# Kernel optimization log

Measured on AMD Instinct MI355X. Metric: run time of the kernel, lower is better.

The kernel has to match this reference:

```python
import jax, jax.numpy as jnp
import numpy as np

B, T, DIM = 4, 2048, 512
H = 8
HD = DIM // H  # 64
ALPHA = 100.0
EPS = 1e-10


def setup_inputs() -> dict:
    key = jax.random.key(0)
    k1, k2, k3, k4 = jax.random.split(key, 4)
    x = jax.random.normal(k1, (B, T, DIM), dtype=jnp.float32)
    # torch Linear weights; stored here as [in, out] for x @ W
    W_qkv = jax.random.normal(k2, (DIM, 2 * DIM), dtype=jnp.float32) * (DIM ** -0.5)
    W_proj = jax.random.normal(k3, (DIM, DIM), dtype=jnp.float32) * (DIM ** -0.5)
    b_proj = jax.random.normal(k4, (DIM,), dtype=jnp.float32) * 0.01
    return {"x": x, "W_qkv": W_qkv, "W_proj": W_proj, "b_proj": b_proj}


def reference(x, W_qkv, W_proj, b_proj):
    b, t, dim = x.shape
    qkv = x @ W_qkv                                   # [b,t,2*dim]
    # einops 'b t (d k h) -> k b h t d' with k=2, h=H: innermost grouping order (d, k, h)
    qkv = qkv.reshape(b, t, HD, 2, H)                 # [b,t,d,2,h]
    qk = jnp.transpose(qkv[:, :, :, 0, :], (0, 3, 1, 2))  # [b,h,t,d]
    v = jnp.transpose(qkv[:, :, :, 1, :], (0, 3, 1, 2))   # [b,h,t,d]
    q = qk  # q == k
    qsq = jnp.sum(q * q, axis=-1)                     # [b,h,t]
    dots = jnp.einsum('bhtd,bhsd->bhts', q, q)        # [b,h,t,s]
    score = -(qsq[..., :, None] + qsq[..., None, :] - 2.0 * dots)
    # Frobenius norm of q over (t,d) per (b,h)
    a = jnp.sqrt(jnp.sum(q * q, axis=(2, 3), keepdims=True))  # [b,h,1,1]
    x_norm = jnp.sqrt(jnp.sum(x * x, axis=-1))                 # [b,t]
    bmax = jnp.max(x_norm, axis=1).reshape(b, 1, 1, 1)         # [b,1,1,1]
    scale = 1.0 / (a * bmax + EPS)
    attn = jax.nn.softmax(ALPHA * score * scale, axis=-1)      # [b,h,t,s]
    out = jnp.einsum('bhts,bhsd->bhtd', attn, v)               # [b,h,t,d]
    out = jnp.transpose(out, (0, 2, 1, 3)).reshape(b, t, dim)  # b t (h d)
    return out @ W_proj + b_proj
```

## Files before the change

kernel.cpp:

```cpp
#include <hip/hip_runtime.h>
#include <hip/hip_bf16.h>

#define BB 4
#define TT 2048
#define DIM 512
#define NH 8
#define HD 64
#define NROW (BB*TT)
#define BH (BB*NH)

typedef unsigned short u16;
typedef unsigned int u32;
typedef __attribute__((ext_vector_type(8))) short bf16x8;
typedef __attribute__((ext_vector_type(8))) unsigned short u16x8;
typedef __attribute__((ext_vector_type(4))) float f32x4;
typedef __attribute__((ext_vector_type(16))) float f32x16;
typedef __attribute__((ext_vector_type(4))) unsigned short u16x4;
typedef __attribute__((ext_vector_type(2))) unsigned int u32x2;

static __device__ __forceinline__ float bf2f(u16 u) {
    return __uint_as_float(((u32)u) << 16);
}
static __device__ __forceinline__ u16 f2bf(float f) {
    u32 u = __float_as_uint(f);
    u32 r = (u + 0x7FFFu + ((u >> 16) & 1u)) >> 16;
    return (u16)r;
}
static __device__ __forceinline__ u32 cvtpk(float a, float b) {
    union { __hip_bfloat162 h2; u32 u; } cv;
    cv.h2 = __float22bfloat162_rn(make_float2(a, b));
    return cv.u;
}
static __device__ __forceinline__ void gll16(const u16* g, u16* l) {
    __builtin_amdgcn_global_load_lds(
        (const __attribute__((address_space(1))) unsigned int*)g,
        (__attribute__((address_space(3))) unsigned int*)l,
        16, 0, 0);
}

__global__ __launch_bounds__(256) void prep_kernel(
    const float* __restrict__ x, u16* __restrict__ x16, u32* __restrict__ bmaxsq,
    const float* __restrict__ Wqkv, u16* __restrict__ Wtq,
    const float* __restrict__ Wproj, u16* __restrict__ Wtp)
{
    const int bid = blockIdx.x;
    const int tid = threadIdx.x;
    __shared__ u16 t[32][33];
    __shared__ float red[4];

    if (bid < 256) {
        const int row = bid * 32 + (tid >> 3);
        const int b = (bid * 32) >> 11;
        const float* xr = x   + (size_t)row * DIM + (tid & 7) * 64;
        u16*        xo  = x16 + (size_t)row * DIM + (tid & 7) * 64;
        float s = 0.0f;
        #pragma unroll
        for (int j = 0; j < 8; ++j) {
            float4 a = *(const float4*)(xr + j*8);
            float4 c = *(const float4*)(xr + j*8 + 4);
            s += a.x*a.x + a.y*a.y + a.z*a.z + a.w*a.w;
            s += c.x*c.x + c.y*c.y + c.z*c.z + c.w*c.w;
            u16x8 pk;
            pk[0]=f2bf(a.x); pk[1]=f2bf(a.y); pk[2]=f2bf(a.z); pk[3]=f2bf(a.w);
            pk[4]=f2bf(c.x); pk[5]=f2bf(c.y); pk[6]=f2bf(c.z); pk[7]=f2bf(c.w);
            *(u16x8*)(xo + j*8) = pk;
        }
        #pragma unroll
        for (int off = 1; off < 8; off <<= 1) s += __shfl_xor(s, off, 64);
        float m = s;
        #pragma unroll
        for (int off = 8; off < 64; off <<= 1) m = fmaxf(m, __shfl_xor(m, off, 64));
        if ((tid & 63) == 0) red[tid >> 6] = m;
        __syncthreads();
        if (tid == 0) {
            float mx = fmaxf(fmaxf(red[0], red[1]), fmaxf(red[2], red[3]));
            atomicMax(&bmaxsq[b], __float_as_uint(mx));
        }
    } else {
        const float* in; u16* outp; int K, N, tb;
        if (bid < 768) { in = Wqkv; outp = Wtq; K = 512; N = 1024; tb = bid - 256; }
        else           { in = Wproj; outp = Wtp; K = 512; N = 512;  tb = bid - 768; }
        const int ntiles = N >> 5;
        const int bx = tb % ntiles, by = tb / ntiles;
        const int n0 = bx * 32, k0 = by * 32;
        const int tx = tid & 31, ty = tid >> 5;
        #pragma unroll
        for (int i = 0; i < 32; i += 8)
            t[ty + i][tx] = f2bf(in[(size_t)(k0 + ty + i) * N + n0 + tx]);
        __syncthreads();
        #pragma unroll
        for (int i = 0; i < 32; i += 8)
            outp[(size_t)(n0 + ty + i) * K + k0 + tx] = t[tx][ty + i];
    }
}

#define LDG 72
__global__ __launch_bounds__(256) void qkv_mfma(
    const u16* __restrict__ x16, const u16* __restrict__ Wt,
    u16* __restrict__ q16, u16* __restrict__ vt16)
{
    const int tid = threadIdx.x, lane = tid & 63, w = tid >> 6;
    const int li = lane & 15, quad = lane >> 4;
    const int mb = blockIdx.x >> 3, nb = blockIdx.x & 7;
    const int row0 = mb * 128, n0 = nb * 128;
    const int b = row0 >> 11;
    const int wm = w >> 1, wn = w & 1;

    __shared__ __align__(16) u16 as[128 * LDG];
    __shared__ __align__(16) u16 bs[128 * LDG];

    f32x4 acc[4][4];
    #pragma unroll
    for (int mi = 0; mi < 4; ++mi)
        #pragma unroll
        for (int ni = 0; ni < 4; ++ni) acc[mi][ni] = f32x4{0.f,0.f,0.f,0.f};

    for (int k0 = 0; k0 < DIM; k0 += 64) {
        __syncthreads();
        #pragma unroll
        for (int it = 0; it < 4; ++it) {
            int id = it * 256 + tid;
            int r = id >> 3, c = id & 7;
            *(bf16x8*)&as[r*LDG + c*8] =
                *(const bf16x8*)(x16 + (size_t)(row0 + r)*DIM + k0 + c*8);
            *(bf16x8*)&bs[r*LDG + c*8] =
                *(const bf16x8*)(Wt  + (size_t)(n0  + r)*DIM + k0 + c*8);
        }
        __syncthreads();

        bf16x8 af[4][2], bfr[4][2];
        #pragma unroll
        for (int mi = 0; mi < 4; ++mi) {
            const u16* p = &as[(wm*64 + mi*16 + li)*LDG + quad*8];
            af[mi][0] = *(const bf16x8*)p;
            af[mi][1] = *(const bf16x8*)(p + 32);
        }
        #pragma unroll
        for (int ni = 0; ni < 4; ++ni) {
            const u16* p = &bs[(wn*64 + ni*16 + li)*LDG + quad*8];
            bfr[ni][0] = *(const bf16x8*)p;
            bfr[ni][1] = *(const bf16x8*)(p + 32);
        }
        #pragma unroll
        for (int mi = 0; mi < 4; ++mi)
            #pragma unroll
            for (int ni = 0; ni < 4; ++ni) {
                acc[mi][ni] = __builtin_amdgcn_mfma_f32_16x16x32_bf16(
                    af[mi][0], bfr[ni][0], acc[mi][ni], 0, 0, 0);
                acc[mi][ni] = __builtin_amdgcn_mfma_f32_16x16x32_bf16(
                    af[mi][1], bfr[ni][1], acc[mi][ni], 0, 0, 0);
            }
    }

    const int h = li & 7;
    const bool isv = ((li >> 3) & 1) != 0;
    #pragma unroll
    for (int ni = 0; ni < 4; ++ni) {
        int col0 = n0 + wn*64 + ni*16;
        int d = col0 >> 4;
        #pragma unroll
        for (int mi = 0; mi < 4; ++mi) {
            int t0 = (row0 & (TT-1)) + wm*64 + mi*16 + quad*4;
            if (!isv) {
                u16* dst = q16 + ((size_t)(b*NH + h)*TT + t0)*HD + d;
                #pragma unroll
                for (int r = 0; r < 4; ++r)
                    dst[(size_t)r * HD] = f2bf(acc[mi][ni][r]);
            } else {
                u16x4 pk;
                pk.x = f2bf(acc[mi][ni][0]); pk.y = f2bf(acc[mi][ni][1]);
                pk.z = f2bf(acc[mi][ni][2]); pk.w = f2bf(acc[mi][ni][3]);
                *(u16x4*)(vt16 + ((size_t)(b*NH + h)*HD + d)*TT + t0) = pk;
            }
        }
    }
}

__global__ __launch_bounds__(256) void proj_mfma(
    const u16* __restrict__ ao16, const u16* __restrict__ Wt,
    const float* __restrict__ bp, float* __restrict__ out)
{
    const int tid = threadIdx.x, lane = tid & 63, w = tid >> 6;
    const int li = lane & 15, quad = lane >> 4;
    const int mb = blockIdx.x >> 2, nb = blockIdx.x & 3;
    const int row0 = mb * 128, n0 = nb * 128;
    const int wm = w >> 1, wn = w & 1;

    __shared__ __align__(16) u16 as[128 * LDG];
    __shared__ __align__(16) u16 bs[128 * LDG];

    f32x4 acc[4][4];
    #pragma unroll
    for (int mi = 0; mi < 4; ++mi)
        #pragma unroll
        for (int ni = 0; ni < 4; ++ni) acc[mi][ni] = f32x4{0.f,0.f,0.f,0.f};

    for (int k0 = 0; k0 < DIM; k0 += 64) {
        __syncthreads();
        #pragma unroll
        for (int it = 0; it < 4; ++it) {
            int id = it * 256 + tid;
            int r = id >> 3, c = id & 7;
            *(bf16x8*)&as[r*LDG + c*8] =
                *(const bf16x8*)(ao16 + (size_t)(row0 + r)*DIM + k0 + c*8);
            *(bf16x8*)&bs[r*LDG + c*8] =
                *(const bf16x8*)(Wt   + (size_t)(n0  + r)*DIM + k0 + c*8);
        }
        __syncthreads();

        bf16x8 af[4][2], bfr[4][2];
        #pragma unroll
        for (int mi = 0; mi < 4; ++mi) {
            const u16* p = &as[(wm*64 + mi*16 + li)*LDG + quad*8];
            af[mi][0] = *(const bf16x8*)p;
            af[mi][1] = *(const bf16x8*)(p + 32);
        }
        #pragma unroll
        for (int ni = 0; ni < 4; ++ni) {
            const u16* p = &bs[(wn*64 + ni*16 + li)*LDG + quad*8];
            bfr[ni][0] = *(const bf16x8*)p;
            bfr[ni][1] = *(const bf16x8*)(p + 32);
        }
        #pragma unroll
        for (int mi = 0; mi < 4; ++mi)
            #pragma unroll
            for (int ni = 0; ni < 4; ++ni) {
                acc[mi][ni] = __builtin_amdgcn_mfma_f32_16x16x32_bf16(
                    af[mi][0], bfr[ni][0], acc[mi][ni], 0, 0, 0);
                acc[mi][ni] = __builtin_amdgcn_mfma_f32_16x16x32_bf16(
                    af[mi][1], bfr[ni][1], acc[mi][ni], 0, 0, 0);
            }
    }

    #pragma unroll
    for (int ni = 0; ni < 4; ++ni) {
        int col = n0 + wn*64 + ni*16 + li;
        float bias = bp[col];
        #pragma unroll
        for (int mi = 0; mi < 4; ++mi) {
            int r0 = row0 + wm*64 + mi*16 + quad*4;
            #pragma unroll
            for (int r = 0; r < 4; ++r)
                out[(size_t)(r0 + r)*DIM + col] = acc[mi][ni][r] + bias;
        }
    }
}

__global__ __launch_bounds__(256) void qsq_kernel(
    const u16* __restrict__ q16, float* __restrict__ qsq, float* __restrict__ asq)
{
    const int tid = threadIdx.x;
    const int bh = blockIdx.x >> 3;
    const int r0 = (blockIdx.x & 7) * 256;
    const u16* qb = q16 + ((size_t)bh * TT + r0) * HD;

    float tot = 0.0f;
    #pragma unroll
    for (int i = 0; i < 8; ++i) {
        int row = i * 32 + (tid >> 3);
        u16x8 v = *(const u16x8*)(qb + (size_t)row * HD + (tid & 7) * 8);
        float s = 0.0f;
        #pragma unroll
        for (int j = 0; j < 8; ++j) { float f = bf2f(v[j]); s += f * f; }
        tot += s;
        #pragma unroll
        for (int off = 1; off < 8; off <<= 1) s += __shfl_xor(s, off, 64);
        if ((tid & 7) == 0) qsq[(size_t)bh * TT + r0 + row] = s;
    }
    __shared__ float red[4];
    #pragma unroll
    for (int off = 32; off > 0; off >>= 1) tot += __shfl_down(tot, off, 64);
    if ((tid & 63) == 0) red[tid >> 6] = tot;
    __syncthreads();
    if (tid == 0) atomicAdd(&asq[bh], red[0] + red[1] + red[2] + red[3]);
}

__global__ __launch_bounds__(256) void attn_kernel(
    const u16* __restrict__ q16, const u16* __restrict__ vt16,
    const float* __restrict__ qsq, const float* __restrict__ asq,
    const u32* __restrict__ bmaxsq, u16* __restrict__ ao16)
{
    const int tid = threadIdx.x;
    const int lane = tid & 63, w = tid >> 6;
    const int l31 = lane & 31, hf = lane >> 5;
    const int l7 = lane & 7;
    const int bh = blockIdx.x >> 4;
    const int qtile = blockIdx.x & 15;
    const int b = bh >> 3, head = bh & 7;

    __shared__ __align__(16) u16 ksA[4][64 * 64];
    __shared__ __align__(16) u16 vtA[4][64 * 64];
    __shared__ __align__(16) float cq[TT];
    __shared__ __align__(16) float invb[4 * 32];

    const u16* qg = q16  + (size_t)bh * TT * HD;
    const u16* vg = vt16 + (size_t)bh * HD * TT;
    const float* qsqg = qsq + (size_t)bh * TT;

    float cf;
    {
        float a  = sqrtf(asq[bh]);
        float bm = sqrtf(__uint_as_float(bmaxsq[b]));
        cf = (100.0f * 1.44269504089f) / (a * bm + 1e-10f);
    }
    const float c2 = 2.0f * cf;

    const int qt0w = qtile * 128 + w * 32;
    bf16x8 qf[4];
    {
        const u16* qrow = qg + (size_t)(qt0w + l31) * HD + hf * 8;
        #pragma unroll
        for (int kc = 0; kc < 4; ++kc)
            qf[kc] = *(const bf16x8*)(qrow + kc * 16);
    }

    const int ci = tid * 8;
    f32x4 cqa = *(const f32x4*)(qsqg + ci);
    f32x4 cqb = *(const f32x4*)(qsqg + ci + 4);

    int slot[4];
    #pragma unroll
    for (int kc = 0; kc < 4; ++kc) slot[kc] = (((2*kc + hf) ^ l7) << 3);

    const int rk = tid >> 3;
    const int ck = (tid & 7) ^ (rk & 7);
    const u16* kstg = qg + (size_t)rk * HD + ck * 8;
    const u16* vstg = vg + (size_t)rk * TT + ck * 8;
    const int lb0 = w * 512;
    const int lb1 = 2048 + w * 512;

    auto stage = [&](int bi, int t) {
        const u16* kp = kstg + (size_t)t * 64 * HD;
        const u16* vp = vstg + t * 64;
        gll16(kp,                 &ksA[bi][0] + lb0);
        gll16(kp + 32 * HD,       &ksA[bi][0] + lb1);
        gll16(vp,                 &vtA[bi][0] + lb0);
        gll16(vp + (size_t)32*TT, &vtA[bi][0] + lb1);
    };

    float ssum = 0.0f;
    f32x16 oacc[2];
    #pragma unroll
    for (int dh = 0; dh < 2; ++dh)
        #pragma unroll
        for (int r = 0; r < 16; ++r) oacc[dh][r] = 0.0f;

    auto tile_compute = [&](const u16* __restrict__ ksb,
                            const u16* __restrict__ vtb, int s0) {
        bf16x8 pa[4];
        #pragma unroll
        for (int sc = 0; sc < 2; ++sc) {
            const u16* kbase = ksb + sc * 2048 + l31 * 64;
            bf16x8 kf0 = *(const bf16x8*)(kbase + slot[0]);
            bf16x8 kf1 = *(const bf16x8*)(kbase + slot[1]);
            bf16x8 kf2 = *(const bf16x8*)(kbase + slot[2]);
            bf16x8 kf3 = *(const bf16x8*)(kbase + slot[3]);
            f32x16 acc;
            #pragma unroll
            for (int r = 0; r < 16; ++r) acc[r] = 0.0f;
            acc = __builtin_amdgcn_mfma_f32_32x32x16_bf16(kf0, qf[0], acc, 0, 0, 0);
            acc = __builtin_amdgcn_mfma_f32_32x32x16_bf16(kf1, qf[1], acc, 0, 0, 0);
            acc = __builtin_amdgcn_mfma_f32_32x32x16_bf16(kf2, qf[2], acc, 0, 0, 0);
            acc = __builtin_amdgcn_mfma_f32_32x32x16_bf16(kf3, qf[3], acc, 0, 0, 0);
            float p[16];
            #pragma unroll
            for (int g = 0; g < 4; ++g) {
                f32x4 cq4 = *(const f32x4*)&cq[s0 + sc*32 + g*8 + hf*4];
                p[4*g+0] = __builtin_amdgcn_exp2f(fmaf(c2, acc[4*g+0], -cq4[0]));
                p[4*g+1] = __builtin_amdgcn_exp2f(fmaf(c2, acc[4*g+1], -cq4[1]));
                p[4*g+2] = __builtin_amdgcn_exp2f(fmaf(c2, acc[4*g+2], -cq4[2]));
                p[4*g+3] = __builtin_amdgcn_exp2f(fmaf(c2, acc[4*g+3], -cq4[3]));
            }
            ssum += (((p[0]+p[1])+(p[2]+p[3])) + ((p[4]+p[5])+(p[6]+p[7])))
                  + (((p[8]+p[9])+(p[10]+p[11])) + ((p[12]+p[13])+(p[14]+p[15])));
            #pragma unroll
            for (int kh = 0; kh < 2; ++kh) {
                u32 A0 = cvtpk(p[8*kh+0], p[8*kh+1]);
                u32 B0 = cvtpk(p[8*kh+4], p[8*kh+5]);
                u32 A1 = cvtpk(p[8*kh+2], p[8*kh+3]);
                u32 B1 = cvtpk(p[8*kh+6], p[8*kh+7]);
                u32x2 r0 = __builtin_amdgcn_permlane32_swap(A0, B0, false, false);
                u32x2 r1 = __builtin_amdgcn_permlane32_swap(A1, B1, false, false);
                union { u32 u[4]; bf16x8 v; } pw;
                pw.u[0] = r0.x; pw.u[1] = r1.x; pw.u[2] = r0.y; pw.u[3] = r1.y;
                pa[sc*2 + kh] = pw.v;
            }
        }
        #pragma unroll
        for (int kc2 = 0; kc2 < 4; ++kc2) {
            #pragma unroll
            for (int dh = 0; dh < 2; ++dh) {
                const u16* vr = vtb + (dh*32 + l31) * 64 + slot[kc2];
                bf16x8 vf = *(const bf16x8*)vr;
                oacc[dh] = __builtin_amdgcn_mfma_f32_32x32x16_bf16(
                    pa[kc2], vf, oacc[dh], 0, 0, 0);
            }
        }
    };

    stage(0, 0); stage(1, 1); stage(2, 2);
    *(f32x4*)&cq[ci]     = cqa * cf;
    *(f32x4*)&cq[ci + 4] = cqb * cf;
    asm volatile("s_waitcnt lgkmcnt(0)" ::: "memory");
    __builtin_amdgcn_s_barrier();

    #pragma unroll 1
    for (int m = 0; m < 7; ++m) {
        const int i0 = m * 4;
        #pragma unroll
        for (int j = 0; j < 4; ++j) {
            asm volatile("s_waitcnt vmcnt(8)" ::: "memory");
            __builtin_amdgcn_s_barrier();
            stage((j + 3) & 3, i0 + j + 3);
            tile_compute(&ksA[j][0], &vtA[j][0], (i0 + j) * 64);
        }
    }
    asm volatile("s_waitcnt vmcnt(8)" ::: "memory");
    __builtin_amdgcn_s_barrier();
    stage(3, 31);
    tile_compute(&ksA[0][0], &vtA[0][0], 28 * 64);
    asm volatile("s_waitcnt vmcnt(8)" ::: "memory");
    __builtin_amdgcn_s_barrier();
    tile_compute(&ksA[1][0], &vtA[1][0], 29 * 64);
    asm volatile("s_waitcnt vmcnt(4)" ::: "memory");
    __builtin_amdgcn_s_barrier();
    tile_compute(&ksA[2][0], &vtA[2][0], 30 * 64);
    asm volatile("s_waitcnt vmcnt(0)" ::: "memory");
    __builtin_amdgcn_s_barrier();
    tile_compute(&ksA[3][0], &vtA[3][0], 31 * 64);

    ssum += __shfl_xor(ssum, 32, 64);
    if (hf == 0) invb[w*32 + l31] = 1.0f / ssum;

    #pragma unroll
    for (int g = 0; g < 4; ++g) {
        f32x4 iv4 = *(const f32x4*)&invb[w*32 + g*8 + hf*4];
        #pragma unroll
        for (int dh = 0; dh < 2; ++dh) {
            #pragma unroll
            for (int r0 = 0; r0 < 4; ++r0) {
                int t = qt0w + g*8 + hf*4 + r0;
                ao16[((size_t)(b*TT + t))*DIM + head*HD + dh*32 + l31] =
                    f2bf(oacc[dh][g*4 + r0] * iv4[r0]);
            }
        }
    }
}

extern "C" void kernel_launch(void* const* d_in, const int* in_sizes, int n_in,
                              void* d_out, int out_size, void* d_ws, size_t ws_size,
                              hipStream_t stream)
{
    const float* x     = (const float*)d_in[0];
    const float* Wqkv  = (const float*)d_in[1];
    const float* Wproj = (const float*)d_in[2];
    const float* bproj = (const float*)d_in[3];
    float* out = (float*)d_out;

    char* ws = (char*)d_ws;
    const size_t MB = 1024*1024;
    u16*   q16  = (u16*)(ws);
    u16*   vt16 = (u16*)(ws + 8*MB);
    u16*   ao16 = (u16*)(ws + 16*MB);
    u16*   x16  = (u16*)(ws + 24*MB);
    u16*   Wtq  = (u16*)(ws + 32*MB);
    u16*   Wtp  = (u16*)(ws + 33*MB);
    float* qsq  = (float*)(ws + 34*MB);
    float* asq  = (float*)(ws + 34*MB + 262144);
    u32* bmaxsq = (u32*)(ws + 34*MB + 262144 + 128);

    (void)in_sizes; (void)n_in; (void)out_size; (void)ws_size;

    hipMemsetAsync(ws + 34*MB + 262144, 0, 144, stream);

    prep_kernel<<<1024, 256, 0, stream>>>(x, x16, bmaxsq, Wqkv, Wtq, Wproj, Wtp);

    qkv_mfma<<<64*8, 256, 0, stream>>>(x16, Wtq, q16, vt16);

    qsq_kernel<<<BH*8, 256, 0, stream>>>(q16, qsq, asq);

    attn_kernel<<<BH*16, 256, 0, stream>>>(q16, vt16, qsq, asq, bmaxsq, ao16);

    proj_mfma<<<64*4, 256, 0, stream>>>(ao16, Wtp, bproj, out);
}
```

Baseline: 136.4 us.

## Split key tiles across wave pairs, each wave handling 64 query rows

```diff
diff --git a/kernel.cpp b/kernel.cpp
--- a/kernel.cpp
+++ b/kernel.cpp
@@ -275,7 +275,7 @@
     if (tid == 0) atomicAdd(&asq[bh], red[0] + red[1] + red[2] + red[3]);
 }
 
-__global__ __launch_bounds__(256) void attn_kernel(
+__global__ __launch_bounds__(256, 2) void attn_kernel(
     const u16* __restrict__ q16, const u16* __restrict__ vt16,
     const float* __restrict__ qsq, const float* __restrict__ asq,
     const u32* __restrict__ bmaxsq, u16* __restrict__ ao16)
@@ -284,17 +284,19 @@
     const int lane = tid & 63, w = tid >> 6;
     const int l31 = lane & 31, hf = lane >> 5;
     const int l7 = lane & 7;
+    const int ws = w & 1;
+    const int p  = w >> 1;
     const int bh = blockIdx.x >> 4;
     const int qtile = blockIdx.x & 15;
     const int b = bh >> 3, head = bh & 7;
 
-    __shared__ __align__(16) u16 ksA[4][64 * 64];
-    __shared__ __align__(16) u16 vtA[4][64 * 64];
-    __shared__ __align__(16) float cq[TT];
-    __shared__ __align__(16) float invb[4 * 32];
-
-    const u16* qg = q16  + (size_t)bh * TT * HD;
-    const u16* vg = vt16 + (size_t)bh * HD * TT;
+    __shared__ __align__(16) u16 smem[36864];
+    u16* ksA = smem;
+    u16* vtA = smem + 16384;
+    float* cq = (float*)(smem + 32768);
+
+    const u16* qgp = q16  + (size_t)bh * TT * HD;
+    const u16* vgp = vt16 + (size_t)bh * HD * TT;
     const float* qsqg = qsq + (size_t)bh * TT;
 
     float cf;
@@ -305,13 +307,14 @@
     }
     const float c2 = 2.0f * cf;
 
-    const int qt0w = qtile * 128 + w * 32;
-    bf16x8 qf[4];
-    {
-        const u16* qrow = qg + (size_t)(qt0w + l31) * HD + hf * 8;
+    const int qt0 = qtile * 128 + p * 64;
+    bf16x8 qf[2][4];
+    #pragma unroll
+    for (int qg = 0; qg < 2; ++qg) {
+        const u16* qrow = qgp + (size_t)(qt0 + qg*32 + l31) * HD + hf * 8;
         #pragma unroll
         for (int kc = 0; kc < 4; ++kc)
-            qf[kc] = *(const bf16x8*)(qrow + kc * 16);
+            qf[qg][kc] = *(const bf16x8*)(qrow + kc * 16);
     }
 
     const int ci = tid * 8;
@@ -324,30 +327,43 @@
 
     const int rk = tid >> 3;
     const int ck = (tid & 7) ^ (rk & 7);
-    const u16* kstg = qg + (size_t)rk * HD + ck * 8;
-    const u16* vstg = vg + (size_t)rk * TT + ck * 8;
+    const u16* kstg = qgp + (size_t)rk * HD + ck * 8;
+    const u16* vstg = vgp + (size_t)rk * TT + ck * 8;
     const int lb0 = w * 512;
     const int lb1 = 2048 + w * 512;
 
-    auto stage = [&](int bi, int t) {
-        const u16* kp = kstg + (size_t)t * 64 * HD;
-        const u16* vp = vstg + t * 64;
-        gll16(kp,                 &ksA[bi][0] + lb0);
-        gll16(kp + 32 * HD,       &ksA[bi][0] + lb1);
-        gll16(vp,                 &vtA[bi][0] + lb0);
-        gll16(vp + (size_t)32*TT, &vtA[bi][0] + lb1);
+    auto stagePair = [&](int sb, int t0g) {
+        #pragma unroll
+        for (int ts = 0; ts < 2; ++ts) {
+            const u16* kp = kstg + (size_t)(t0g + ts) * 64 * HD;
+            const u16* vp = vstg + (t0g + ts) * 64;
+            u16* kb = ksA + (sb + ts) * 4096;
+            u16* vb = vtA + (sb + ts) * 4096;
+            gll16(kp,                 kb + lb0);
+            gll16(kp + 32 * HD,       kb + lb1);
+            gll16(vp,                 vb + lb0);
+            gll16(vp + (size_t)32*TT, vb + lb1);
+        }
     };
 
-    float ssum = 0.0f;
-    f32x16 oacc[2];
-    #pragma unroll
-    for (int dh = 0; dh < 2; ++dh)
-        #pragma unroll
-        for (int r = 0; r < 16; ++r) oacc[dh][r] = 0.0f;
+    bf16x8 onesf;
+    {
+        union { u16 a[8]; bf16x8 v; } o;
+        #pragma unroll
+        for (int i = 0; i < 8; ++i) o.a[i] = 0x3F80;
+        onesf = o.v;
+    }
+
+    f32x16 oacc[2][2], osum[2];
+    #pragma unroll
+    for (int qg = 0; qg < 2; ++qg) {
+        #pragma unroll
+        for (int r = 0; r < 16; ++r) { oacc[qg][0][r] = 0.f; oacc[qg][1][r] = 0.f; osum[qg][r] = 0.f; }
+    }
 
     auto tile_compute = [&](const u16* __restrict__ ksb,
                             const u16* __restrict__ vtb, int s0) {
-        bf16x8 pa[4];
+        bf16x8 pa[2][4];
         #pragma unroll
         for (int sc = 0; sc < 2; ++sc) {
             const u16* kbase = ksb + sc * 2048 + l31 * 64;
@@ -355,94 +371,132 @@
             bf16x8 kf1 = *(const bf16x8*)(kbase + slot[1]);
             bf16x8 kf2 = *(const bf16x8*)(kbase + slot[2]);
             bf16x8 kf3 = *(const bf16x8*)(kbase + slot[3]);
-            f32x16 acc;
-            #pragma unroll
-            for (int r = 0; r < 16; ++r) acc[r] = 0.0f;
-            acc = __builtin_amdgcn_mfma_f32_32x32x16_bf16(kf0, qf[0], acc, 0, 0, 0);
-            acc = __builtin_amdgcn_mfma_f32_32x32x16_bf16(kf1, qf[1], acc, 0, 0, 0);
-            acc = __builtin_amdgcn_mfma_f32_32x32x16_bf16(kf2, qf[2], acc, 0, 0, 0);
-            acc = __builtin_amdgcn_mfma_f32_32x32x16_bf16(kf3, qf[3], acc, 0, 0, 0);
-            float p[16];
-            #pragma unroll
-            for (int g = 0; g < 4; ++g) {
-                f32x4 cq4 = *(const f32x4*)&cq[s0 + sc*32 + g*8 + hf*4];
-                p[4*g+0] = __builtin_amdgcn_exp2f(fmaf(c2, acc[4*g+0], -cq4[0]));
-                p[4*g+1] = __builtin_amdgcn_exp2f(fmaf(c2, acc[4*g+1], -cq4[1]));
-                p[4*g+2] = __builtin_amdgcn_exp2f(fmaf(c2, acc[4*g+2], -cq4[2]));
-                p[4*g+3] = __builtin_amdgcn_exp2f(fmaf(c2, acc[4*g+3], -cq4[3]));
+            f32x4 cq4[4];
+            #pragma unroll
+            for (int g = 0; g < 4; ++g)
+                cq4[g] = *(const f32x4*)&cq[s0 + sc*32 + g*8 + hf*4];
+            #pragma unroll
+            for (int qg = 0; qg < 2; ++qg) {
+                f32x16 acc;
+                #pragma unroll
+                for (int r = 0; r < 16; ++r) acc[r] = 0.0f;
+                __builtin_amdgcn_s_setprio(1);
+                acc = __builtin_amdgcn_mfma_f32_32x32x16_bf16(kf0, qf[qg][0], acc, 0, 0, 0);
+                acc = __builtin_amdgcn_mfma_f32_32x32x16_bf16(kf1, qf[qg][1], acc, 0, 0, 0);
+                acc = __builtin_amdgcn_mfma_f32_32x32x16_bf16(kf2, qf[qg][2], acc, 0, 0, 0);
+                acc = __builtin_amdgcn_mfma_f32_32x32x16_bf16(kf3, qf[qg][3], acc, 0, 0, 0);
+                __builtin_amdgcn_s_setprio(0);
+                float pv[16];
+                #pragma unroll
+                for (int g = 0; g < 4; ++g) {
+                    pv[4*g+0] = __builtin_amdgcn_exp2f(fmaf(c2, acc[4*g+0], -cq4[g][0]));
+                    pv[4*g+1] = __builtin_amdgcn_exp2f(fmaf(c2, acc[4*g+1], -cq4[g][1]));
+                    pv[4*g+2] = __builtin_amdgcn_exp2f(fmaf(c2, acc[4*g+2], -cq4[g][2]));
+                    pv[4*g+3] = __builtin_amdgcn_exp2f(fmaf(c2, acc[4*g+3], -cq4[g][3]));
+                }
+                #pragma unroll
+                for (int kh = 0; kh < 2; ++kh) {
+                    u32 A0 = cvtpk(pv[8*kh+0], pv[8*kh+1]);
+                    u32 B0 = cvtpk(pv[8*kh+4], pv[8*kh+5]);
+                    u32 A1 = cvtpk(pv[8*kh+2], pv[8*kh+3]);
+                    u32 B1 = cvtpk(pv[8*kh+6], pv[8*kh+7]);
+                    u32x2 r0 = __builtin_amdgcn_permlane32_swap(A0, B0, false, false);
+                    u32x2 r1 = __builtin_amdgcn_permlane32_swap(A1, B1, false, false);
+                    union { u32 u[4]; bf16x8 v; } pw;
+                    pw.u[0] = r0.x; pw.u[1] = r1.x; pw.u[2] = r0.y; pw.u[3] = r1.y;
+                    pa[qg][sc*2 + kh] = pw.v;
+                }
             }
-            ssum += (((p[0]+p[1])+(p[2]+p[3])) + ((p[4]+p[5])+(p[6]+p[7])))
-                  + (((p[8]+p[9])+(p[10]+p[11])) + ((p[12]+p[13])+(p[14]+p[15])));
-            #pragma unroll
-            for (int kh = 0; kh < 2; ++kh) {
-                u32 A0 = cvtpk(p[8*kh+0], p[8*kh+1]);
-                u32 B0 = cvtpk(p[8*kh+4], p[8*kh+5]);
-                u32 A1 = cvtpk(p[8*kh+2], p[8*kh+3]);
-                u32 B1 = cvtpk(p[8*kh+6], p[8*kh+7]);
-                u32x2 r0 = __builtin_amdgcn_permlane32_swap(A0, B0, false, false);
-                u32x2 r1 = __builtin_amdgcn_permlane32_swap(A1, B1, false, false);
-                union { u32 u[4]; bf16x8 v; } pw;
-                pw.u[0] = r0.x; pw.u[1] = r1.x; pw.u[2] = r0.y; pw.u[3] = r1.y;
-                pa[sc*2 + kh] = pw.v;
+        }
+        #pragma unroll
+        for (int kc = 0; kc < 4; ++kc) {
+            bf16x8 vf0 = *(const bf16x8*)(vtb + (0*32 + l31) * 64 + slot[kc]);
+            bf16x8 vf1 = *(const bf16x8*)(vtb + (1*32 + l31) * 64 + slot[kc]);
+            __builtin_amdgcn_s_setprio(1);
+            #pragma unroll
+            for (int qg = 0; qg < 2; ++qg) {
+                oacc[qg][0] = __builtin_amdgcn_mfma_f32_32x32x16_bf16(
+                    pa[qg][kc], vf0, oacc[qg][0], 0, 0, 0);
+                oacc[qg][1] = __builtin_amdgcn_mfma_f32_32x32x16_bf16(
+                    pa[qg][kc], vf1, oacc[qg][1], 0, 0, 0);
+                osum[qg] = __builtin_amdgcn_mfma_f32_32x32x16_bf16(
+                    pa[qg][kc], onesf, osum[qg], 0, 0, 0);
             }
-        }
-        #pragma unroll
-        for (int kc2 = 0; kc2 < 4; ++kc2) {
-            #pragma unroll
-            for (int dh = 0; dh < 2; ++dh) {
-                const u16* vr = vtb + (dh*32 + l31) * 64 + slot[kc2];
-                bf16x8 vf = *(const bf16x8*)vr;
-                oacc[dh] = __builtin_amdgcn_mfma_f32_32x32x16_bf16(
-                    pa[kc2], vf, oacc[dh], 0, 0, 0);
-            }
+            __builtin_amdgcn_s_setprio(0);
         }
     };
 
-    stage(0, 0); stage(1, 1); stage(2, 2);
+    stagePair(0, 0);
+    stagePair(2, 2);
     *(f32x4*)&cq[ci]     = cqa * cf;
     *(f32x4*)&cq[ci + 4] = cqb * cf;
     asm volatile("s_waitcnt lgkmcnt(0)" ::: "memory");
     __builtin_amdgcn_s_barrier();
 
-    #pragma unroll 1
-    for (int m = 0; m < 7; ++m) {
-        const int i0 = m * 4;
-        #pragma unroll
-        for (int j = 0; j < 4; ++j) {
-            asm volatile("s_waitcnt vmcnt(8)" ::: "memory");
-            __builtin_amdgcn_s_barrier();
-            stage((j + 3) & 3, i0 + j + 3);
-            tile_compute(&ksA[j][0], &vtA[j][0], (i0 + j) * 64);
-        }
-    }
-    asm volatile("s_waitcnt vmcnt(8)" ::: "memory");
-    __builtin_amdgcn_s_barrier();
-    stage(3, 31);
-    tile_compute(&ksA[0][0], &vtA[0][0], 28 * 64);
-    asm volatile("s_waitcnt vmcnt(8)" ::: "memory");
-    __builtin_amdgcn_s_barrier();
-    tile_compute(&ksA[1][0], &vtA[1][0], 29 * 64);
-    asm volatile("s_waitcnt vmcnt(4)" ::: "memory");
-    __builtin_amdgcn_s_barrier();
-    tile_compute(&ksA[2][0], &vtA[2][0], 30 * 64);
+    #pragma unroll 2
+    for (int m = 0; m < 15; ++m) {
+        asm volatile("s_waitcnt vmcnt(8)" ::: "memory");
+        __builtin_amdgcn_s_barrier();
+        const int sb = (m & 1) * 2;
+        tile_compute(ksA + (sb + ws) * 4096, vtA + (sb + ws) * 4096,
+                     (2*m + ws) * 64);
+        __builtin_amdgcn_s_barrier();
+        if (m <= 13) stagePair(sb, 2*(m + 2));
+    }
     asm volatile("s_waitcnt vmcnt(0)" ::: "memory");
     __builtin_amdgcn_s_barrier();
-    tile_compute(&ksA[3][0], &vtA[3][0], 31 * 64);
-
-    ssum += __shfl_xor(ssum, 32, 64);
-    if (hf == 0) invb[w*32 + l31] = 1.0f / ssum;
-
-    #pragma unroll
-    for (int g = 0; g < 4; ++g) {
-        f32x4 iv4 = *(const f32x4*)&invb[w*32 + g*8 + hf*4];
-        #pragma unroll
-        for (int dh = 0; dh < 2; ++dh) {
-            #pragma unroll
-            for (int r0 = 0; r0 < 4; ++r0) {
-                int t = qt0w + g*8 + hf*4 + r0;
-                ao16[((size_t)(b*TT + t))*DIM + head*HD + dh*32 + l31] =
-                    f2bf(oacc[dh][g*4 + r0] * iv4[r0]);
-            }
+    tile_compute(ksA + (2 + ws) * 4096, vtA + (2 + ws) * 4096,
+                 (30 + ws) * 64);
+    __builtin_amdgcn_s_barrier();
+
+    float* cmb = (float*)smem;
+    float* myc = cmb + p * 6144 + lane * 96;
+    if (ws == 1) {
+        #pragma unroll
+        for (int qg = 0; qg < 2; ++qg) {
+            #pragma unroll
+            for (int dh = 0; dh < 2; ++dh)
+                #pragma unroll
+                for (int v4 = 0; v4 < 4; ++v4)
+                    *(f32x4*)(myc + (qg*2 + dh)*16 + v4*4) =
+                        f32x4{oacc[qg][dh][v4*4+0], oacc[qg][dh][v4*4+1],
+                              oacc[qg][dh][v4*4+2], oacc[qg][dh][v4*4+3]};
+            #pragma unroll
+            for (int v4 = 0; v4 < 4; ++v4)
+                *(f32x4*)(myc + 64 + qg*16 + v4*4) =
+                    f32x4{osum[qg][v4*4+0], osum[qg][v4*4+1],
+                          osum[qg][v4*4+2], osum[qg][v4*4+3]};
+        }
+    }
+    asm volatile("s_waitcnt lgkmcnt(0)" ::: "memory");
+    __builtin_amdgcn_s_barrier();
+    if (ws == 0) {
+        #pragma unroll
+        for (int qg = 0; qg < 2; ++qg) {
+            #pragma unroll
+            for (int dh = 0; dh < 2; ++dh)
+                #pragma unroll
+                for (int r = 0; r < 16; ++r)
+                    oacc[qg][dh][r] += myc[(qg*2 + dh)*16 + r];
+            #pragma unroll
+            for (int r = 0; r < 16; ++r)
+                osum[qg][r] += myc[64 + qg*16 + r];
+        }
+        #pragma unroll
+        for (int qg = 0; qg < 2; ++qg) {
+            float inv[16];
+            #pragma unroll
+            for (int r = 0; r < 16; ++r) inv[r] = 1.0f / osum[qg][r];
+            #pragma unroll
+            for (int dh = 0; dh < 2; ++dh)
+                #pragma unroll
+                for (int g = 0; g < 4; ++g)
+                    #pragma unroll
+                    for (int r0 = 0; r0 < 4; ++r0) {
+                        int t = qt0 + qg*32 + g*8 + hf*4 + r0;
+                        ao16[((size_t)(b*TT + t))*DIM + head*HD + dh*32 + l31] =
+                            f2bf(oacc[qg][dh][g*4 + r0] * inv[g*4 + r0]);
+                    }
         }
     }
 }
```

Result: faster. 132.8 us (-2.6%).
